# Kernel tuning notes

Hardware: AMD Instinct MI355X
Metric: run time of the kernel (lower is better)

## Reference

```python
import jax, jax.numpy as jnp
import numpy as np

KH, KW = 5, 5               # kernel_size from init_kwargs
PAD_H, PAD_W = (KH - 1) // 2, (KW - 1) // 2
MED_IDX = (KH * KW - 1) // 2  # torch.median -> lower median; exact middle for odd counts


def setup_inputs() -> dict:
    key = jax.random.key(0)
    x = jax.random.normal(key, (2, 4, 1024, 1024), dtype=jnp.float32)  # B,C,H,W
    return {"x": x}


def reference(x):
    # Zero-pad spatially, matching F.conv2d(padding=(k-1)//2), stride=1.
    B, C, H, W = x.shape
    xp = jnp.pad(x, ((0, 0), (0, 0), (PAD_H, PAD_H), (PAD_W, PAD_W)))
    # Extract K*K shifted views (equivalent to the binary grouped conv2d),
    # stacked into [B, C, KH*KW, H, W] — same layout as features.view(b,c,-1,h,w).
    patches = jnp.stack(
        [xp[:, :, i:i + H, j:j + W] for i in range(KH) for j in range(KW)],
        axis=2,
    )
    # torch.median(dim=2)[0]: sort the window axis and take the middle element.
    return jnp.sort(patches, axis=2)[:, :, MED_IDX]
```

## Files before the change

kernel.cpp:

```cpp
#include <hip/hip_runtime.h>

#define IMG_W 1024
#define IMG_H 1024

typedef _Float16 h2 __attribute__((ext_vector_type(2)));

__device__ __forceinline__ h2 mn(h2 a, h2 b) { return __builtin_elementwise_min(a, b); }
__device__ __forceinline__ h2 mx(h2 a, h2 b) { return __builtin_elementwise_max(a, b); }
__device__ __forceinline__ void ce(h2 &a, h2 &b) { h2 t = mn(a, b); b = mx(a, b); a = t; }
__device__ __forceinline__ h2 med3p(h2 a, h2 b, h2 c) {
    return mx(mn(a, b), mn(mx(a, b), c));
}
__device__ __forceinline__ void sort5(h2 &a0, h2 &a1, h2 &a2, h2 &a3, h2 &a4) {
    ce(a0, a1); ce(a3, a4); ce(a2, a4); ce(a2, a3);
    ce(a0, a3); ce(a0, a2); ce(a1, a4); ce(a1, a3); ce(a1, a2);
}
__device__ __forceinline__ void sort4(h2 &a, h2 &b, h2 &c, h2 &d) {
    ce(a, b); ce(c, d); ce(a, c); ce(b, d); ce(b, c);
}

__device__ __forceinline__ h2 bch2(unsigned u) { return __builtin_bit_cast(h2, u); }

struct Row { h2 a, b, c, d, e; };

__device__ __forceinline__ Row load_sort_row(const unsigned* __restrict__ ldsrow, int tx) {
    unsigned d0 = ldsrow[tx], d1 = ldsrow[tx + 1], d2 = ldsrow[tx + 2];
    h2 p0 = bch2(d0);
    h2 p1 = bch2((d0 >> 16) | (d1 << 16));
    h2 p2 = bch2(d1);
    h2 p3 = bch2((d1 >> 16) | (d2 << 16));
    h2 p4 = bch2(d2);
    sort5(p0, p1, p2, p3, p4);
    return {p0, p1, p2, p3, p4};
}

__device__ __forceinline__ h2 tail13(h2 A, h2 B, h2 c1a, h2 c1b, h2 c1c,
                                     h2 c2a, h2 c2b, h2 c2c,
                                     h2 c3a, h2 c3b, h2 c3c, h2 D, h2 E) {
    ce(A, D); ce(c1a, c3a); ce(A, c1a);
    ce(B, E); ce(c1b, c3b); ce(E, c3b);
    h2 e0 = B, e1 = D, e2 = E, e3 = c1a, e4 = c1b, e5 = c3a, e6 = c1c;
    ce(e0, e1); ce(e2, e3); ce(e4, e5);
    ce(e0, e2); ce(e4, e6); ce(e0, e4);
    ce(e1, e3); ce(e5, e6); ce(e3, e6);
    h2 f0 = e1, f1 = e2, f2 = e3, f3 = e4, f4 = e5, f5 = c2a;
    ce(f0, f1); ce(f2, f3); ce(f4, f5);
    ce(f0, f2); ce(f0, f4);
    ce(f1, f3); ce(f3, f5);
    h2 g0 = f1, g1 = f2, g2 = f3, g3 = f4, g4 = c2b;
    ce(g0, g1); ce(g2, g3);
    ce(g0, g2); ce(g0, g4);
    ce(g1, g3); ce(g3, g4);
    h2 h0 = g1, h1 = g2, h2_ = g3, h3 = c2c;
    ce(h0, h1); ce(h2_, h3); ce(h0, h2_); ce(h1, h3);
    return med3p(h1, h2_, c3c);
}

__device__ __forceinline__ void pair_medians(const Row &rb, const Row &rc, const Row &rd,
                                             const Row &re, const Row &ra, const Row &rf,
                                             h2 &out_lo, h2 &out_hi) {
    h2 s0, s1, s2, s3;
    s0 = rb.a; s1 = rc.a; s2 = rd.a; s3 = re.a; sort4(s0, s1, s2, s3);
    h2 Bl = mx(s3, ra.a), Al = mx(s2, mn(s3, ra.a));
    h2 Bh = mx(s3, rf.a), Ah = mx(s2, mn(s3, rf.a));
    s0 = rb.b; s1 = rc.b; s2 = rd.b; s3 = re.b; sort4(s0, s1, s2, s3);
    h2 c1al = s2, c1bl = s3, c1cl = mx(s1, ra.b);
    h2 c1ah = s2, c1bh = s3, c1ch = mx(s1, rf.b);
    s0 = rb.c; s1 = rc.c; s2 = rd.c; s3 = re.c; sort4(s0, s1, s2, s3);
    h2 c2al = s1, c2bl = s2, c2cl = med3p(s0, ra.c, s3);
    h2 c2ah = s1, c2bh = s2, c2ch = med3p(s0, rf.c, s3);
    s0 = rb.d; s1 = rc.d; s2 = rd.d; s3 = re.d; sort4(s0, s1, s2, s3);
    h2 c3al = s0, c3bl = s1, c3cl = mn(s2, ra.d);
    h2 c3ah = s0, c3bh = s1, c3ch = mn(s2, rf.d);
    s0 = rb.e; s1 = rc.e; s2 = rd.e; s3 = re.e; sort4(s0, s1, s2, s3);
    h2 Dl = mn(s0, ra.e), El = mn(s1, mx(s0, ra.e));
    h2 Dh = mn(s0, rf.e), Eh = mn(s1, mx(s0, rf.e));

    out_lo = tail13(Al, Bl, c1al, c1bl, c1cl, c2al, c2bl, c2cl, c3al, c3bl, c3cl, Dl, El);
    out_hi = tail13(Ah, Bh, c1ah, c1bh, c1ch, c2ah, c2bh, c2ch, c3ah, c3bh, c3ch, Dh, Eh);
}

#define LDS_DW 35
__global__ __launch_bounds__(256, 4) void median5x5_kernel(const float* __restrict__ x,
                                                           float* __restrict__ out) {
    __shared__ unsigned lds[68][LDS_DW];

    const int tx = threadIdx.x;
    const int ty = threadIdx.y;
    const int tid = ty * 32 + tx;
    const int plane = blockIdx.z;
    const float* src = x + (size_t)plane * IMG_H * IMG_W;

    const int gx0 = blockIdx.x * 64 - 2;
    const int gy0 = blockIdx.y * 64 - 2;

    for (unsigned idx = tid; idx < 68u * LDS_DW; idx += 256) {
        unsigned r = idx / LDS_DW;
        unsigned dc = idx - r * LDS_DW;
        int gy = gy0 + (int)r;
        int gxa = gx0 + 2 * (int)dc;
        int gxb = gxa + 1;
        bool rowok = (unsigned)gy < (unsigned)IMG_H;
        float a = (rowok && (unsigned)gxa < (unsigned)IMG_W) ? src[gy * IMG_W + gxa] : 0.0f;
        float b = (rowok && (unsigned)gxb < (unsigned)IMG_W) ? src[gy * IMG_W + gxb] : 0.0f;
        lds[r][dc] = __builtin_bit_cast(unsigned, __builtin_amdgcn_cvt_pkrtz(a, b));
    }
    __syncthreads();

    const int base = ty * 8;
    Row S0 = load_sort_row(&lds[base + 0][0], tx);
    Row S1 = load_sort_row(&lds[base + 1][0], tx);
    Row S2 = load_sort_row(&lds[base + 2][0], tx);
    Row S3 = load_sort_row(&lds[base + 3][0], tx);
    Row S4 = load_sort_row(&lds[base + 4][0], tx);
    Row S5 = load_sort_row(&lds[base + 5][0], tx);

    float* dst = out + (size_t)plane * IMG_H * IMG_W
               + (size_t)(blockIdx.y * 64 + base) * IMG_W + blockIdx.x * 64 + 2 * tx;
    h2 mlo, mhi;

#define EMIT(vv, m) do {                                                       \
        float2 o; o.x = (float)(m).x; o.y = (float)(m).y;                      \
        *reinterpret_cast<float2*>(dst + (size_t)(vv) * IMG_W) = o;            \
    } while (0)

    pair_medians(S1, S2, S3, S4, S0, S5, mlo, mhi);
    EMIT(0, mlo); EMIT(1, mhi);
    S0 = load_sort_row(&lds[base + 6][0], tx);
    S1 = load_sort_row(&lds[base + 7][0], tx);
    pair_medians(S3, S4, S5, S0, S2, S1, mlo, mhi);
    EMIT(2, mlo); EMIT(3, mhi);
    S2 = load_sort_row(&lds[base + 8][0], tx);
    S3 = load_sort_row(&lds[base + 9][0], tx);
    pair_medians(S5, S0, S1, S2, S4, S3, mlo, mhi);
    EMIT(4, mlo); EMIT(5, mhi);
    S4 = load_sort_row(&lds[base + 10][0], tx);
    S5 = load_sort_row(&lds[base + 11][0], tx);
    pair_medians(S1, S2, S3, S4, S0, S5, mlo, mhi);
    EMIT(6, mlo); EMIT(7, mhi);
#undef EMIT
}

extern "C" void kernel_launch(void* const* d_in, const int* in_sizes, int n_in,
                              void* d_out, int out_size, void* d_ws, size_t ws_size,
                              hipStream_t stream) {
    const float* x = (const float*)d_in[0];
    float* out = (float*)d_out;
    const int planes = in_sizes[0] / (IMG_H * IMG_W);
    dim3 grid(IMG_W / 64, IMG_H / 64, planes);
    dim3 block(32, 8);
    median5x5_kernel<<<grid, block, 0, stream>>>(x, out);
}
```

Baseline: 96.88 us.

## Load rows directly from global memory instead of staging tiles in LDS

Drops the shared-memory tile and the __syncthreads barrier. Each thread now reads its 6-float row windows straight from global memory with float2 loads and packs them to fp16 in registers. The block shape changes to 64x4 threads covering 128x32 output tiles. Only the left and right edge blocks use a per-element clamped path. This removes the LDS staging pass and barrier, at the cost of redundant global and L2 reads for overlapping halo rows and columns, and more pack conversions per thread.

```diff
diff --git a/kernel.cpp b/kernel.cpp
--- a/kernel.cpp
+++ b/kernel.cpp
@@ -11,6 +11,9 @@
 __device__ __forceinline__ h2 med3p(h2 a, h2 b, h2 c) {
     return mx(mn(a, b), mn(mx(a, b), c));
 }
+__device__ __forceinline__ h2 pkrtz(float a, float b) {
+    return __builtin_bit_cast(h2, __builtin_amdgcn_cvt_pkrtz(a, b));
+}
 __device__ __forceinline__ void sort5(h2 &a0, h2 &a1, h2 &a2, h2 &a3, h2 &a4) {
     ce(a0, a1); ce(a3, a4); ce(a2, a4); ce(a2, a3);
     ce(a0, a3); ce(a0, a2); ce(a1, a4); ce(a1, a3); ce(a1, a2);
@@ -19,19 +22,33 @@
     ce(a, b); ce(c, d); ce(a, c); ce(b, d); ce(b, c);
 }
 
-__device__ __forceinline__ h2 bch2(unsigned u) { return __builtin_bit_cast(h2, u); }
-
 struct Row { h2 a, b, c, d, e; };
 
-__device__ __forceinline__ Row load_sort_row(const unsigned* __restrict__ ldsrow, int tx) {
-    unsigned d0 = ldsrow[tx], d1 = ldsrow[tx + 1], d2 = ldsrow[tx + 2];
-    h2 p0 = bch2(d0);
-    h2 p1 = bch2((d0 >> 16) | (d1 << 16));
-    h2 p2 = bch2(d1);
-    h2 p3 = bch2((d1 >> 16) | (d2 << 16));
-    h2 p4 = bch2(d2);
+__device__ __forceinline__ Row make_row(float w0, float w1, float w2,
+                                        float w3, float w4, float w5) {
+    h2 p0 = pkrtz(w0, w1), p1 = pkrtz(w1, w2), p2 = pkrtz(w2, w3),
+       p3 = pkrtz(w3, w4), p4 = pkrtz(w4, w5);
     sort5(p0, p1, p2, p3, p4);
     return {p0, p1, p2, p3, p4};
+}
+
+__device__ __forceinline__ Row load_row_i(const float* __restrict__ rowp, int gcx) {
+    float2 f01 = *reinterpret_cast<const float2*>(rowp + gcx - 2);
+    float2 f23 = *reinterpret_cast<const float2*>(rowp + gcx);
+    float2 f45 = *reinterpret_cast<const float2*>(rowp + gcx + 2);
+    return make_row(f01.x, f01.y, f23.x, f23.y, f45.x, f45.y);
+}
+
+__device__ __forceinline__ Row load_row_e(const float* __restrict__ rowp, int gcx) {
+    float w[6];
+    #pragma unroll
+    for (int j = 0; j < 6; ++j) {
+        int c = gcx - 2 + j;
+        int cc = min(max(c, 0), IMG_W - 1);
+        float v = rowp[cc];
+        w[j] = ((unsigned)c < (unsigned)IMG_W) ? v : 0.0f;
+    }
+    return make_row(w[0], w[1], w[2], w[3], w[4], w[5]);
 }
 
 __device__ __forceinline__ h2 tail13(h2 A, h2 B, h2 c1a, h2 c1b, h2 c1c,
@@ -80,43 +97,30 @@
     out_hi = tail13(Ah, Bh, c1ah, c1bh, c1ch, c2ah, c2bh, c2ch, c3ah, c3bh, c3ch, Dh, Eh);
 }
 
-#define LDS_DW 35
 __global__ __launch_bounds__(256, 4) void median5x5_kernel(const float* __restrict__ x,
                                                            float* __restrict__ out) {
-    __shared__ unsigned lds[68][LDS_DW];
-
     const int tx = threadIdx.x;
     const int ty = threadIdx.y;
-    const int tid = ty * 32 + tx;
+    const int bx = blockIdx.x;
+    const int by = blockIdx.y;
     const int plane = blockIdx.z;
     const float* src = x + (size_t)plane * IMG_H * IMG_W;
 
-    const int gx0 = blockIdx.x * 64 - 2;
-    const int gy0 = blockIdx.y * 64 - 2;
+    const int gcx = bx * 128 + 2 * tx;
+    const int row0 = by * 32 + ty * 8;
+    const bool eblk = (bx == 0) | (bx == 7);
 
-    for (unsigned idx = tid; idx < 68u * LDS_DW; idx += 256) {
-        unsigned r = idx / LDS_DW;
-        unsigned dc = idx - r * LDS_DW;
-        int gy = gy0 + (int)r;
-        int gxa = gx0 + 2 * (int)dc;
-        int gxb = gxa + 1;
-        bool rowok = (unsigned)gy < (unsigned)IMG_H;
-        float a = (rowok && (unsigned)gxa < (unsigned)IMG_W) ? src[gy * IMG_W + gxa] : 0.0f;
-        float b = (rowok && (unsigned)gxb < (unsigned)IMG_W) ? src[gy * IMG_W + gxb] : 0.0f;
-        lds[r][dc] = __builtin_bit_cast(unsigned, __builtin_amdgcn_cvt_pkrtz(a, b));
-    }
-    __syncthreads();
+    const h2 z = {(_Float16)0, (_Float16)0};
+    const Row ZR = {z, z, z, z, z};
 
-    const int base = ty * 8;
-    Row S0 = load_sort_row(&lds[base + 0][0], tx);
-    Row S1 = load_sort_row(&lds[base + 1][0], tx);
-    Row S2 = load_sort_row(&lds[base + 2][0], tx);
-    Row S3 = load_sort_row(&lds[base + 3][0], tx);
-    Row S4 = load_sort_row(&lds[base + 4][0], tx);
-    Row S5 = load_sort_row(&lds[base + 5][0], tx);
+#define LROW(gy_) ( ((unsigned)(gy_) >= (unsigned)IMG_H) ? ZR                  \
+                    : (eblk ? load_row_e(src + (size_t)(gy_) * IMG_W, gcx)     \
+                            : load_row_i(src + (size_t)(gy_) * IMG_W, gcx)) )
 
-    float* dst = out + (size_t)plane * IMG_H * IMG_W
-               + (size_t)(blockIdx.y * 64 + base) * IMG_W + blockIdx.x * 64 + 2 * tx;
+    Row S0 = LROW(row0 - 2), S1 = LROW(row0 - 1), S2 = LROW(row0 + 0),
+        S3 = LROW(row0 + 1), S4 = LROW(row0 + 2), S5 = LROW(row0 + 3);
+
+    float* dst = out + (size_t)plane * IMG_H * IMG_W + (size_t)row0 * IMG_W + gcx;
     h2 mlo, mhi;
 
 #define EMIT(vv, m) do {                                                       \
@@ -126,19 +130,17 @@
 
     pair_medians(S1, S2, S3, S4, S0, S5, mlo, mhi);
     EMIT(0, mlo); EMIT(1, mhi);
-    S0 = load_sort_row(&lds[base + 6][0], tx);
-    S1 = load_sort_row(&lds[base + 7][0], tx);
+    S0 = LROW(row0 + 4); S1 = LROW(row0 + 5);
     pair_medians(S3, S4, S5, S0, S2, S1, mlo, mhi);
     EMIT(2, mlo); EMIT(3, mhi);
-    S2 = load_sort_row(&lds[base + 8][0], tx);
-    S3 = load_sort_row(&lds[base + 9][0], tx);
+    S2 = LROW(row0 + 6); S3 = LROW(row0 + 7);
     pair_medians(S5, S0, S1, S2, S4, S3, mlo, mhi);
     EMIT(4, mlo); EMIT(5, mhi);
-    S4 = load_sort_row(&lds[base + 10][0], tx);
-    S5 = load_sort_row(&lds[base + 11][0], tx);
+    S4 = LROW(row0 + 8); S5 = LROW(row0 + 9);
     pair_medians(S1, S2, S3, S4, S0, S5, mlo, mhi);
     EMIT(6, mlo); EMIT(7, mhi);
 #undef EMIT
+#undef LROW
 }
 
 extern "C" void kernel_launch(void* const* d_in, const int* in_sizes, int n_in,
@@ -147,7 +149,7 @@
     const float* x = (const float*)d_in[0];
     float* out = (float*)d_out;
     const int planes = in_sizes[0] / (IMG_H * IMG_W);
-    dim3 grid(IMG_W / 64, IMG_H / 64, planes);
-    dim3 block(32, 8);
+    dim3 grid(IMG_W / 128, IMG_H / 32, planes);
+    dim3 block(64, 4);
     median5x5_kernel<<<grid, block, 0, stream>>>(x, out);
 }
```

Result: slower. 99.03 us (+2.2%).
